# Optimization experiments

Measured on AMD Instinct MI355X. Metric: run time of the kernel, lower is better.

The kernel has to match this reference:

```python
import jax, jax.numpy as jnp
import numpy as np

NBODY = 63          # body 0 = world, body 1 = free-joint root, bodies 2..62 = hinge
NHINGE = NBODY - 2  # 61 hinge dofs -> qpos dim = 7 + 61 = 68
NSITES = 16
B = 131072


def _qmul(q1, q2):
    """Hamilton product, (w,x,y,z) convention. Broadcasts over leading dims."""
    w1, x1, y1, z1 = q1[..., 0], q1[..., 1], q1[..., 2], q1[..., 3]
    w2, x2, y2, z2 = q2[..., 0], q2[..., 1], q2[..., 2], q2[..., 3]
    return jnp.stack([
        w1 * w2 - x1 * x2 - y1 * y2 - z1 * z2,
        w1 * x2 + x1 * w2 + y1 * z2 - z1 * y2,
        w1 * y2 - x1 * z2 + y1 * w2 + z1 * x2,
        w1 * z2 + x1 * y2 - y1 * x2 + z1 * w2,
    ], axis=-1)


def _qrot(q, v):
    """Rotate v by unit quaternion q (equivalent to q*v*q^-1 sandwich)."""
    u = q[..., 1:]
    w = q[..., :1]
    t = 2.0 * jnp.cross(u, v)
    return v + w * t + jnp.cross(u, t)


def setup_inputs() -> dict:
    key = jax.random.key(0)
    ks = jax.random.split(key, 8)
    qpos = jax.random.normal(ks[0], (B, 7 + NHINGE), dtype=jnp.float32) * 0.3
    body_pos = jax.random.normal(ks[1], (NBODY, 3), dtype=jnp.float32) * 0.1
    bq = jax.random.normal(ks[2], (NBODY, 4), dtype=jnp.float32)
    body_quat = bq / jnp.linalg.norm(bq, axis=-1, keepdims=True)
    ax = jax.random.normal(ks[3], (NHINGE, 3), dtype=jnp.float32)
    hinge_axis = ax / jnp.linalg.norm(ax, axis=-1, keepdims=True)
    jnt_pos = jax.random.normal(ks[4], (NHINGE, 3), dtype=jnp.float32) * 0.05
    site_pos = jax.random.normal(ks[5], (NSITES, 3), dtype=jnp.float32) * 0.05
    body_parent = jnp.maximum(jnp.arange(NBODY, dtype=jnp.int32) - 1, 0)  # chain tree
    site_body = jax.random.randint(ks[6], (NSITES,), 1, NBODY, dtype=jnp.int32)
    return {
        'qpos': qpos, 'body_pos': body_pos, 'body_quat': body_quat,
        'hinge_axis': hinge_axis, 'jnt_pos': jnt_pos, 'site_pos': site_pos,
        'body_parent': body_parent, 'site_body': site_body,
    }


def reference(qpos, body_pos, body_quat, hinge_axis, jnt_pos, site_pos,
              body_parent, site_body):
    # Structural ints are static tree topology: pull to host for Python indexing.
    parents = np.asarray(body_parent)
    sbody = np.asarray(site_body)
    Bn = qpos.shape[0]
    nbody = body_pos.shape[0]

    wp = [None] * nbody  # per-body world position [B,3]
    wq = [None] * nbody  # per-body world quaternion [B,4]
    wp[0] = jnp.zeros((Bn, 3), dtype=qpos.dtype)
    wq[0] = jnp.broadcast_to(jnp.array([1.0, 0.0, 0.0, 0.0], dtype=qpos.dtype), (Bn, 4))

    # body 1: free joint -> root pos + normalized quat straight from qpos
    wp[1] = qpos[:, 0:3]
    q = qpos[:, 3:7]
    wq[1] = q / jnp.linalg.norm(q, axis=-1, keepdims=True)

    # hinge bodies, parents always processed before children
    for bid in range(2, nbody):
        h = bid - 2
        p = int(parents[bid])
        half = 0.5 * qpos[:, 7 + h]
        s, c = jnp.sin(half), jnp.cos(half)
        ax = hinge_axis[h]
        hq = jnp.stack([c, s * ax[0], s * ax[1], s * ax[2]], axis=-1)  # [B,4]
        local_combined = _qmul(jnp.broadcast_to(body_quat[bid], (Bn, 4)), hq)
        anchor = wp[p] + _qrot(wq[p], body_pos[bid] + jnt_pos[h])  # world joint anchor
        nq = _qmul(wq[p], local_combined)
        wq[bid] = nq
        wp[bid] = anchor - _qrot(nq, jnt_pos[h])

    WP = jnp.stack(wp, axis=1)  # [B, nbody, 3]
    WQ = jnp.stack(wq, axis=1)  # [B, nbody, 4]

    # sites: vectorized gather + rotate over all keypoint sites at once
    sq = WQ[:, sbody]                         # [B, S, 4]
    sp = WP[:, sbody]                         # [B, S, 3]
    sites = sp + _qrot(sq, site_pos[None, :, :])  # [B, S, 3]
    return sites
```

## Files before the change

kernel.cpp:

```cpp
#include <hip/hip_runtime.h>


#define NBODY  63
#define NHINGE 61
#define NSITES 16
#define QDIM   68
#define LSTRIDE 49

__global__ __launch_bounds__(256, 2)
void fk_main(const float* __restrict__ qpos,
             const float* __restrict__ body_pos,
             const float* __restrict__ body_quat,
             const float* __restrict__ hinge_axis,
             const float* __restrict__ jnt_pos,
             const float* __restrict__ site_pos,
             const int* __restrict__ site_body,
             float* __restrict__ out, int nb)
{
    __shared__ float sbuf[256 * LSTRIDE];
    __shared__ float hc[NHINGE][16];
    __shared__ float spos[NSITES][4];
    __shared__ int   smask[NBODY];

    const int tid = threadIdx.x;
    const int t = blockIdx.x * 256 + tid;
    float* my = sbuf + tid * LSTRIDE;

    float f[QDIM];
    if (t < nb) {
        const float4* q4 = reinterpret_cast<const float4*>(qpos) + (size_t)t * 17;
#pragma unroll
        for (int i = 0; i < 17; i++) {
            float4 v = q4[i];
            f[4*i+0] = v.x; f[4*i+1] = v.y; f[4*i+2] = v.z; f[4*i+3] = v.w;
        }
    }
    __builtin_amdgcn_sched_barrier(0);

    if (tid < NHINGE) {
        int h = tid, bid = h + 2;
        float uw = body_quat[bid*4+0], ux = body_quat[bid*4+1];
        float uy = body_quat[bid*4+2], uz = body_quat[bid*4+3];
        float ax = hinge_axis[h*3+0], ay = hinge_axis[h*3+1], az = hinge_axis[h*3+2];
        float jx = jnt_pos[h*3+0],   jy = jnt_pos[h*3+1],   jz = jnt_pos[h*3+2];
        float bx = body_pos[bid*3+0], by = body_pos[bid*3+1], bz = body_pos[bid*3+2];
        hc[h][0] = uw; hc[h][1] = ux; hc[h][2] = uy; hc[h][3] = uz;
        hc[h][4] = -(ux * ax + uy * ay + uz * az);
        hc[h][5] =  uw * ax + uy * az - uz * ay;
        hc[h][6] =  uw * ay - ux * az + uz * ax;
        hc[h][7] =  uw * az + ux * ay - uy * ax;
        hc[h][8] = bx + jx; hc[h][9] = by + jy; hc[h][10] = bz + jz; hc[h][11] = 0.f;
        hc[h][12] = jx; hc[h][13] = jy; hc[h][14] = jz; hc[h][15] = 0.f;
    }
    if (tid < NSITES) {
        spos[tid][0] = site_pos[tid*3+0];
        spos[tid][1] = site_pos[tid*3+1];
        spos[tid][2] = site_pos[tid*3+2];
        spos[tid][3] = 0.f;
    }
    if (tid < NBODY) {
        int m = 0;
#pragma unroll
        for (int s = 0; s < NSITES; s++)
            m |= (site_body[s] == tid) ? (1 << s) : 0;
        smask[tid] = m;
    }
    unsigned long long bodymask = 0ull;
#pragma unroll
    for (int s = 0; s < NSITES; s++)
        bodymask |= 1ull << site_body[s];

    __syncthreads();

    if (t < nb) {
        float wpx = f[0], wpy = f[1], wpz = f[2];
        float qw = f[3], qx = f[4], qy = f[5], qz = f[6];
        float inv = rsqrtf(qw * qw + qx * qx + qy * qy + qz * qz);
        qw *= inv; qx *= inv; qy *= inv; qz *= inv;

        auto emit = [&](int bid) {
            int m = smask[bid];
            while (m) {
                int s = __ffs(m) - 1; m &= m - 1;
                float vx = spos[s][0], vy = spos[s][1], vz = spos[s][2];
                float tx = 2.f * (qy * vz - qz * vy);
                float ty = 2.f * (qz * vx - qx * vz);
                float tz = 2.f * (qx * vy - qy * vx);
                float* o = my + s * 3;
                o[0] = wpx + vx + qw * tx + (qy * tz - qz * ty);
                o[1] = wpy + vy + qw * ty + (qz * tx - qx * tz);
                o[2] = wpz + vz + qw * tz + (qx * ty - qy * tx);
            }
        };

        if (bodymask & 2ull) emit(1);

#pragma unroll
        for (int h = 0; h < NHINGE; h++) {
            const int bid = h + 2;
            const float* c = hc[h];
            float ang = 0.5f * f[7 + h];
            float sn, cs;
            __sincosf(ang, &sn, &cs);
            float lw = cs * c[0] + sn * c[4];
            float lx = cs * c[1] + sn * c[5];
            float ly = cs * c[2] + sn * c[6];
            float lz = cs * c[3] + sn * c[7];
            float ax = c[8], ay = c[9], az = c[10];
            float tx = 2.f * (qy * az - qz * ay);
            float ty = 2.f * (qz * ax - qx * az);
            float tz = 2.f * (qx * ay - qy * ax);
            float anx = wpx + ax + qw * tx + (qy * tz - qz * ty);
            float any_ = wpy + ay + qw * ty + (qz * tx - qx * tz);
            float anz = wpz + az + qw * tz + (qx * ty - qy * tx);
            float nw = qw * lw - qx * lx - qy * ly - qz * lz;
            float nx = qw * lx + qx * lw + qy * lz - qz * ly;
            float ny = qw * ly - qx * lz + qy * lw + qz * lx;
            float nz = qw * lz + qx * ly - qy * lx + qz * lw;
            float jx = c[12], jy = c[13], jz = c[14];
            float t2x = 2.f * (ny * jz - nz * jy);
            float t2y = 2.f * (nz * jx - nx * jz);
            float t2z = 2.f * (nx * jy - ny * jx);
            wpx = anx - (jx + nw * t2x + (ny * t2z - nz * t2y));
            wpy = any_ - (jy + nw * t2y + (nz * t2x - nx * t2z));
            wpz = anz - (jz + nw * t2z + (nx * t2y - ny * t2x));
            qw = nw; qx = nx; qy = ny; qz = nz;

            if (bodymask & (1ull << bid)) emit(bid);
        }
    }

    __syncthreads();

    {
        size_t blk_dw = (size_t)blockIdx.x * (256 * 48);
        if (blk_dw + 256 * 48 <= (size_t)nb * 48) {
            float4* out4 = reinterpret_cast<float4*>(out + blk_dw);
#pragma unroll
            for (int k = 0; k < 12; k++) {
                int g = k * 256 + tid;
                int q = g / 12;
                int r = (g - q * 12) * 4;
                const float* p = sbuf + q * LSTRIDE + r;
                float4 v = { p[0], p[1], p[2], p[3] };
                out4[g] = v;
            }
        } else if (t < nb) {
            for (int k = 0; k < 48; k++) out[(size_t)t * 48 + k] = my[k];
        }
    }
}

extern "C" void kernel_launch(void* const* d_in, const int* in_sizes, int n_in,
                              void* d_out, int out_size, void* d_ws, size_t ws_size,
                              hipStream_t stream)
{
    const float* qpos       = (const float*)d_in[0];
    const float* body_pos   = (const float*)d_in[1];
    const float* body_quat  = (const float*)d_in[2];
    const float* hinge_axis = (const float*)d_in[3];
    const float* jnt_pos    = (const float*)d_in[4];
    const float* site_pos   = (const float*)d_in[5];
    const int* site_body    = (const int*)d_in[7];

    int nb = in_sizes[0] / QDIM;

    fk_main<<<(nb + 255) / 256, 256, 0, stream>>>(qpos, body_pos, body_quat,
                                                  hinge_axis, jnt_pos, site_pos,
                                                  site_body, (float*)d_out, nb);
}
```

Measured before the change: 121.1 us.

## Stage qpos through LDS with coalesced loads, keep site outputs in registers

The kernel now copies each block's qpos rows into a padded LDS tile with coalesced float4 loads, and each thread reads its joint angles from that tile. The old LDS staging of outputs is removed: the 48 site outputs stay in registers and each thread writes its own row directly as float4 stores. The hinge loop changes from full unroll to unroll-by-2, and site emission compares against a register copy of site_body instead of an LDS bitmask. The aim is cheaper input loads and fewer LDS round trips, at the cost of strided per-thread output stores, higher register pressure and a larger LDS footprint per block.

```diff
diff --git a/kernel.cpp b/kernel.cpp
--- a/kernel.cpp
+++ b/kernel.cpp
@@ -4,8 +4,11 @@
 #define NBODY  63
 #define NHINGE 61
 #define NSITES 16
-#define QDIM   68
-#define LSTRIDE 49
+#define QDIM    68
+#define QSTRIDE 69
+#define EPB    256
+
+typedef unsigned long long u64;
 
 __global__ __launch_bounds__(256, 2)
 void fk_main(const float* __restrict__ qpos,
@@ -15,27 +18,14 @@
              const float* __restrict__ jnt_pos,
              const float* __restrict__ site_pos,
              const int* __restrict__ site_body,
-             float* __restrict__ out, int nb)
+             float* __restrict__ out, int nenv)
 {
-    __shared__ float sbuf[256 * LSTRIDE];
+    __shared__ float qt[EPB * QSTRIDE];
     __shared__ float hc[NHINGE][16];
     __shared__ float spos[NSITES][4];
-    __shared__ int   smask[NBODY];
 
     const int tid = threadIdx.x;
-    const int t = blockIdx.x * 256 + tid;
-    float* my = sbuf + tid * LSTRIDE;
-
-    float f[QDIM];
-    if (t < nb) {
-        const float4* q4 = reinterpret_cast<const float4*>(qpos) + (size_t)t * 17;
-#pragma unroll
-        for (int i = 0; i < 17; i++) {
-            float4 v = q4[i];
-            f[4*i+0] = v.x; f[4*i+1] = v.y; f[4*i+2] = v.z; f[4*i+3] = v.w;
-        }
-    }
-    __builtin_amdgcn_sched_barrier(0);
+    const int t   = blockIdx.x * EPB + tid;
 
     if (tid < NHINGE) {
         int h = tid, bid = h + 2;
@@ -58,50 +48,66 @@
         spos[tid][2] = site_pos[tid*3+2];
         spos[tid][3] = 0.f;
     }
-    if (tid < NBODY) {
-        int m = 0;
+
+    int sbody[NSITES];
 #pragma unroll
-        for (int s = 0; s < NSITES; s++)
-            m |= (site_body[s] == tid) ? (1 << s) : 0;
-        smask[tid] = m;
+    for (int s = 0; s < NSITES; s++) sbody[s] = site_body[s];
+    u64 bodymask = 0ull;
+#pragma unroll
+    for (int s = 0; s < NSITES; s++) bodymask |= 1ull << sbody[s];
+
+    const bool fullblk = ((size_t)(blockIdx.x + 1) * EPB <= (size_t)nenv);
+    if (fullblk) {
+        const float4* src = reinterpret_cast<const float4*>(qpos)
+                          + (size_t)blockIdx.x * (EPB * 17);
+#pragma unroll
+        for (int i = 0; i < 17; i++) {
+            int g = i * EPB + tid;
+            float4 v = src[g];
+            int e = g / 17;
+            int c = g - e * 17;
+            float* d = qt + e * QSTRIDE + c * 4;
+            d[0] = v.x; d[1] = v.y; d[2] = v.z; d[3] = v.w;
+        }
+    } else if (t < nenv) {
+        const float* src = qpos + (size_t)t * QDIM;
+        for (int i = 0; i < QDIM; i++) qt[tid * QSTRIDE + i] = src[i];
     }
-    unsigned long long bodymask = 0ull;
-#pragma unroll
-    for (int s = 0; s < NSITES; s++)
-        bodymask |= 1ull << site_body[s];
-
     __syncthreads();
 
-    if (t < nb) {
-        float wpx = f[0], wpy = f[1], wpz = f[2];
-        float qw = f[3], qx = f[4], qy = f[5], qz = f[6];
-        float inv = rsqrtf(qw * qw + qx * qx + qy * qy + qz * qz);
+    float o[48];
+
+    if (t < nenv) {
+        const float* q = qt + tid * QSTRIDE;
+
+        float wpx = q[0], wpy = q[1], wpz = q[2];
+        float qw = q[3], qx = q[4], qy = q[5], qz = q[6];
+        float inv = rsqrtf(qw*qw + qx*qx + qy*qy + qz*qz);
         qw *= inv; qx *= inv; qy *= inv; qz *= inv;
 
-        auto emit = [&](int bid) {
-            int m = smask[bid];
-            while (m) {
-                int s = __ffs(m) - 1; m &= m - 1;
-                float vx = spos[s][0], vy = spos[s][1], vz = spos[s][2];
-                float tx = 2.f * (qy * vz - qz * vy);
-                float ty = 2.f * (qz * vx - qx * vz);
-                float tz = 2.f * (qx * vy - qy * vx);
-                float* o = my + s * 3;
-                o[0] = wpx + vx + qw * tx + (qy * tz - qz * ty);
-                o[1] = wpy + vy + qw * ty + (qz * tx - qx * tz);
-                o[2] = wpz + vz + qw * tz + (qx * ty - qy * tx);
+        auto emitBody = [&](int bid) {
+#pragma unroll
+            for (int s = 0; s < NSITES; s++) {
+                if (sbody[s] == bid) {
+                    float vx = spos[s][0], vy = spos[s][1], vz = spos[s][2];
+                    float tx = 2.f * (qy * vz - qz * vy);
+                    float ty = 2.f * (qz * vx - qx * vz);
+                    float tz = 2.f * (qx * vy - qy * vx);
+                    o[3*s+0] = wpx + vx + qw * tx + (qy * tz - qz * ty);
+                    o[3*s+1] = wpy + vy + qw * ty + (qz * tx - qx * tz);
+                    o[3*s+2] = wpz + vz + qw * tz + (qx * ty - qy * tx);
+                }
             }
         };
 
-        if (bodymask & 2ull) emit(1);
+        if (bodymask & 2ull) emitBody(1);
 
-#pragma unroll
-        for (int h = 0; h < NHINGE; h++) {
-            const int bid = h + 2;
+#pragma clang loop unroll_count(2)
+        for (int h = 0; h < NHINGE; ++h) {
+            float ang = q[7 + h];
             const float* c = hc[h];
-            float ang = 0.5f * f[7 + h];
             float sn, cs;
-            __sincosf(ang, &sn, &cs);
+            __sincosf(0.5f * ang, &sn, &cs);
             float lw = cs * c[0] + sn * c[4];
             float lx = cs * c[1] + sn * c[5];
             float ly = cs * c[2] + sn * c[6];
@@ -126,27 +132,15 @@
             wpz = anz - (jz + nw * t2z + (nx * t2y - ny * t2x));
             qw = nw; qx = nx; qy = ny; qz = nz;
 
-            if (bodymask & (1ull << bid)) emit(bid);
+            int bid = h + 2;
+            if ((bodymask >> bid) & 1ull) emitBody(bid);
         }
-    }
 
-    __syncthreads();
-
-    {
-        size_t blk_dw = (size_t)blockIdx.x * (256 * 48);
-        if (blk_dw + 256 * 48 <= (size_t)nb * 48) {
-            float4* out4 = reinterpret_cast<float4*>(out + blk_dw);
+        float4* o4 = reinterpret_cast<float4*>(out + (size_t)t * 48);
 #pragma unroll
-            for (int k = 0; k < 12; k++) {
-                int g = k * 256 + tid;
-                int q = g / 12;
-                int r = (g - q * 12) * 4;
-                const float* p = sbuf + q * LSTRIDE + r;
-                float4 v = { p[0], p[1], p[2], p[3] };
-                out4[g] = v;
-            }
-        } else if (t < nb) {
-            for (int k = 0; k < 48; k++) out[(size_t)t * 48 + k] = my[k];
+        for (int i = 0; i < 12; i++) {
+            float4 v = { o[4*i+0], o[4*i+1], o[4*i+2], o[4*i+3] };
+            o4[i] = v;
         }
     }
 }
@@ -163,9 +157,9 @@
     const float* site_pos   = (const float*)d_in[5];
     const int* site_body    = (const int*)d_in[7];
 
-    int nb = in_sizes[0] / QDIM;
+    int nenv = in_sizes[0] / QDIM;
 
-    fk_main<<<(nb + 255) / 256, 256, 0, stream>>>(qpos, body_pos, body_quat,
-                                                  hinge_axis, jnt_pos, site_pos,
-                                                  site_body, (float*)d_out, nb);
+    fk_main<<<(nenv + EPB - 1) / EPB, EPB, 0, stream>>>(qpos, body_pos, body_quat,
+                                                        hinge_axis, jnt_pos, site_pos,
+                                                        site_body, (float*)d_out, nenv);
 }
```

Result: slower. 128.9 us (+6.5%).
